# Performance work log

Hardware: AMD Instinct MI355X
Metric: run time of the kernel (lower is better)

The kernel has to match this reference:

```python
import jax, jax.numpy as jnp
import numpy as np

B, S, HID, H = 2, 2048, 1024, 16
D = HID // H
ROTARY_BASE = 10000.0
LN_EPS = 1e-5
NEG = -1e9


def setup_inputs() -> dict:
    key = jax.random.key(0)
    ks = jax.random.split(key, 20)
    w = lambda k, shape: (jax.random.normal(k, shape, jnp.float32) * 0.02)
    return {
        "x": jax.random.normal(ks[0], (B, S, HID), jnp.float32),
        "mask": jnp.ones((B, S), jnp.int32),
        "wq": w(ks[1], (HID, HID)), "bq": jnp.zeros((HID,), jnp.float32),
        "wk": w(ks[2], (HID, HID)), "bk": jnp.zeros((HID,), jnp.float32),
        "wv": w(ks[3], (HID, HID)), "bv": jnp.zeros((HID,), jnp.float32),
        "wo": w(ks[4], (HID, HID)), "bo": jnp.zeros((HID,), jnp.float32),
        "w1": w(ks[5], (HID, 4 * HID)), "b1": jnp.zeros((4 * HID,), jnp.float32),
        "w2": w(ks[6], (4 * HID, HID)), "b2": jnp.zeros((HID,), jnp.float32),
        "ln1_g": jnp.ones((HID,), jnp.float32), "ln1_b": jnp.zeros((HID,), jnp.float32),
        "ln2_g": jnp.ones((HID,), jnp.float32), "ln2_b": jnp.zeros((HID,), jnp.float32),
    }


def _layer_norm(z, g, b):
    m = z.mean(-1, keepdims=True)
    v = ((z - m) ** 2).mean(-1, keepdims=True)
    return (z - m) / jnp.sqrt(v + LN_EPS) * g + b


def _rope(t, cos, sin):
    # t: [B,H,S,D]; even/odd halves rotated then CONCATENATED (matches source, not interleaved)
    e, o = t[..., 0::2], t[..., 1::2]
    return jnp.concatenate([e * cos - o * sin, e * sin + o * cos], axis=-1)


def reference(x, mask, wq, bq, wk, bk, wv, bv, wo, bo, w1, b1, w2, b2,
              ln1_g, ln1_b, ln2_g, ln2_b):
    b, s, hid = x.shape
    h, d = H, D
    # rotary tables for positions [0, s)
    inv_freq = 1.0 / (ROTARY_BASE ** (jnp.arange(0, d, 2, dtype=jnp.float32) / d))
    freqs = jnp.arange(s, dtype=jnp.float32)[:, None] * inv_freq[None, :]  # [S, D/2]
    cos = jnp.cos(freqs)[None, None]  # [1,1,S,D/2]
    sin = jnp.sin(freqs)[None, None]

    # ---- attention sublayer (pre-norm) ----
    xn = _layer_norm(x, ln1_g, ln1_b)
    q = (xn @ wq + bq).reshape(b, s, h, d).transpose(0, 2, 1, 3)
    k = (xn @ wk + bk).reshape(b, s, h, d).transpose(0, 2, 1, 3)
    v = (xn @ wv + bv).reshape(b, s, h, d).transpose(0, 2, 1, 3)
    q = _rope(q, cos, sin)
    k = _rope(k, cos, sin)

    scores = jnp.einsum('bhqd,bhkd->bhqk', q, k) / np.sqrt(d).astype(np.float32)
    pad = (mask == 0)[:, None, None, :]              # [B,1,1,S]
    scores = jnp.where(pad, NEG, scores)
    causal = jnp.triu(jnp.ones((s, s), bool), 1)     # [S,S]
    scores = jnp.where(causal, NEG, scores)
    probs = jax.nn.softmax(scores, axis=-1)          # dropout p=0.0 (eval)
    ctx = jnp.einsum('bhqk,bhkd->bhqd', probs, v)
    ctx = ctx.transpose(0, 2, 1, 3).reshape(b, s, hid)
    attn_out = ctx @ wo + bo
    x = x + attn_out

    # ---- FFN sublayer (pre-norm) ----
    xn = _layer_norm(x, ln2_g, ln2_b)
    f = jax.nn.gelu(xn @ w1 + b1, approximate=True) @ w2 + b2
    return x + f
```

## Files before the change

### kernel.cpp

```cpp
#include <hip/hip_runtime.h>

typedef unsigned short u16;
typedef unsigned int u32;
typedef __attribute__((ext_vector_type(8))) u16 u16x8;
typedef __attribute__((ext_vector_type(4))) u16 u16x4;
typedef __attribute__((ext_vector_type(8))) __bf16 bf16x8;
typedef __attribute__((ext_vector_type(4))) float f32x4;

static __device__ __forceinline__ float bf2f(u16 u) {
    union { u32 i; float f; } v; v.i = ((u32)u) << 16; return v.f;
}
static __device__ __forceinline__ u16 f2bf(float f) {
    union { float f; u32 i; } v; v.f = f;
    u32 r = v.i + 0x7fffu + ((v.i >> 16) & 1u);
    return (u16)(r >> 16);
}
static __device__ __forceinline__ u16 f2bfn(float f) {
    __bf16 h = (__bf16)f;
    return *(u16*)&h;
}
static __device__ __forceinline__ void gl_lds16(const void* gsrc, void* ldst) {
    __builtin_amdgcn_global_load_lds((const __attribute__((address_space(1))) void*)gsrc,
                                     (__attribute__((address_space(3))) void*)ldst, 16, 0, 0);
}

__global__ __launch_bounds__(256) void transpose_cvt(const float* __restrict__ in,
                                                     u16* __restrict__ out, int K, int N) {
    __shared__ float t[32][33];
    int k0 = blockIdx.y << 5, n0 = blockIdx.x << 5;
    int r = threadIdx.x >> 3, c4 = threadIdx.x & 7;
    float4 v = *(const float4*)(in + (size_t)(k0 + r) * N + n0 + (c4 << 2));
    t[r][c4 * 4 + 0] = v.x; t[r][c4 * 4 + 1] = v.y;
    t[r][c4 * 4 + 2] = v.z; t[r][c4 * 4 + 3] = v.w;
    __syncthreads();
    u16x4 o;
    o[0] = f2bf(t[c4 * 4 + 0][r]); o[1] = f2bf(t[c4 * 4 + 1][r]);
    o[2] = f2bf(t[c4 * 4 + 2][r]); o[3] = f2bf(t[c4 * 4 + 3][r]);
    *(u16x4*)(out + (size_t)(n0 + r) * K + k0 + (c4 << 2)) = o;
}

__global__ void concat_bias(const float* __restrict__ bq, const float* __restrict__ bk,
                            const float* __restrict__ bv, float* __restrict__ bqkv) {
    int i = blockIdx.x * 256 + threadIdx.x;
    if (i < 3072) {
        float v = (i < 1024) ? bq[i] : (i < 2048 ? bk[i - 1024] : bv[i - 2048]);
        bqkv[i] = v;
    }
}

__global__ void rope_tab(float* __restrict__ cost, float* __restrict__ sint) {
    int idx = blockIdx.x * 256 + threadIdx.x;
    int s = idx >> 5, f = idx & 31;
    float inv = powf(10000.0f, -((float)(2 * f)) / 64.0f);
    float a = (float)s * inv;
    cost[idx] = cosf(a);
    sint[idx] = sinf(a);
}

__global__ __launch_bounds__(256) void ln_kernel(const float* __restrict__ x,
                                                 const float* __restrict__ gam,
                                                 const float* __restrict__ bet,
                                                 u16* __restrict__ out) {
    int row = blockIdx.x, tid = threadIdx.x;
    float4 v = *((const float4*)(x + (size_t)row * 1024) + tid);
    float s = v.x + v.y + v.z + v.w;
    float sq = v.x * v.x + v.y * v.y + v.z * v.z + v.w * v.w;
    #pragma unroll
    for (int off = 32; off >= 1; off >>= 1) {
        s += __shfl_xor(s, off);
        sq += __shfl_xor(sq, off);
    }
    __shared__ float red[8];
    int wid = tid >> 6, lane = tid & 63;
    if (lane == 0) { red[wid] = s; red[wid + 4] = sq; }
    __syncthreads();
    float ts = red[0] + red[1] + red[2] + red[3];
    float tq = red[4] + red[5] + red[6] + red[7];
    float mean = ts * (1.0f / 1024.0f);
    float var = tq * (1.0f / 1024.0f) - mean * mean;
    float rstd = rsqrtf(var + 1e-5f);
    float4 g = ((const float4*)gam)[tid];
    float4 b = ((const float4*)bet)[tid];
    u16x4 o;
    o[0] = f2bfn((v.x - mean) * rstd * g.x + b.x);
    o[1] = f2bfn((v.y - mean) * rstd * g.y + b.y);
    o[2] = f2bfn((v.z - mean) * rstd * g.z + b.z);
    o[3] = f2bfn((v.w - mean) * rstd * g.w + b.w);
    *(u16x4*)(out + (size_t)row * 1024 + (tid << 2)) = o;
}

template <int EPI>
__global__ __launch_bounds__(256) void gemm_bt(const u16* __restrict__ A, const u16* __restrict__ Bt,
                                               const float* __restrict__ bias,
                                               const float* __restrict__ res,
                                               u16* __restrict__ outb, float* __restrict__ outf,
                                               float* __restrict__ pout,
                                               int M, int N, int K) {
    __shared__ __align__(16) u16 As[3][4096];
    __shared__ __align__(16) u16 Bs[3][4096];
    const int tid = threadIdx.x;
    const int lane = tid & 63, wid = tid >> 6;
    const int g = lane >> 4, cl = lane & 15;
    const int wr = wid >> 1, wc = wid & 1;
    const int gx = gridDim.x;
    const int lid = blockIdx.y * gx + blockIdx.x;
    const int per8 = (gx * gridDim.y) >> 3;
    const int newlin = (lid & 7) * per8 + (lid >> 3);
    const int m0 = (newlin / gx) << 7;
    const int n0 = (newlin % gx) << 7;
    const int kchunk = K / gridDim.z;
    const int kbase = blockIdx.z * kchunk;
    const int NT = kchunk >> 5;
    f32x4 acc[4][4] = {};
    const int grow = tid >> 2;
    const int gcol = (tid & 3) ^ ((tid >> 3) & 3);

    auto stage = [&](int buf, int kt) {
        const int ko = kbase + (kt << 5);
        gl_lds16(A + (size_t)(m0 + grow) * K + ko + (gcol << 3),       &As[buf][wid << 9]);
        gl_lds16(A + (size_t)(m0 + grow + 64) * K + ko + (gcol << 3),  &As[buf][(wid << 9) + 2048]);
        gl_lds16(Bt + (size_t)(n0 + grow) * K + ko + (gcol << 3),      &Bs[buf][wid << 9]);
        gl_lds16(Bt + (size_t)(n0 + grow + 64) * K + ko + (gcol << 3), &Bs[buf][(wid << 9) + 2048]);
    };

    stage(0, 0);
    stage(1, 1);
    for (int kt = 0; kt < NT; ++kt) {
        if (kt + 1 < NT) asm volatile("s_waitcnt vmcnt(4)" ::: "memory");
        else             asm volatile("s_waitcnt vmcnt(0)" ::: "memory");
        __builtin_amdgcn_s_barrier();
        __builtin_amdgcn_sched_barrier(0);
        if (kt + 2 < NT) stage((kt + 2) % 3, kt + 2);
        const int cb = kt % 3;
        bf16x8 a[4], b[4];
        #pragma unroll
        for (int i = 0; i < 4; ++i) {
            int row = (wr << 6) + (i << 4) + cl;
            a[i] = *(const bf16x8*)&As[cb][((row << 2) + (g ^ ((row >> 1) & 3))) << 3];
        }
        #pragma unroll
        for (int j = 0; j < 4; ++j) {
            int row = (wc << 6) + (j << 4) + cl;
            b[j] = *(const bf16x8*)&Bs[cb][((row << 2) + (g ^ ((row >> 1) & 3))) << 3];
        }
        __builtin_amdgcn_s_setprio(1);
        #pragma unroll
        for (int i = 0; i < 4; ++i)
            #pragma unroll
            for (int j = 0; j < 4; ++j)
                acc[i][j] = __builtin_amdgcn_mfma_f32_16x16x32_bf16(a[i], b[j], acc[i][j], 0, 0, 0);
        __builtin_amdgcn_s_setprio(0);
    }
    if (blockIdx.z == 0) {
        #pragma unroll
        for (int i = 0; i < 4; ++i)
            #pragma unroll
            for (int j = 0; j < 4; ++j) {
                int row = m0 + (wr << 6) + (i << 4) + (g << 2);
                int col = n0 + (wc << 6) + (j << 4) + cl;
                float bc = bias[col];
                #pragma unroll
                for (int rr = 0; rr < 4; ++rr) {
                    float v = acc[i][j][rr] + bc;
                    size_t idx = (size_t)(row + rr) * N + col;
                    if constexpr (EPI == 0) {
                        outb[idx] = f2bfn(v);
                    } else if constexpr (EPI == 1) {
                        outf[idx] = v + res[idx];
                    } else {
                        float t = 0.7978845608f * (v + 0.044715f * v * v * v);
                        outb[idx] = f2bfn(v / (1.0f + exp2f(t * -2.88539008f)));
                    }
                }
            }
    } else {
        #pragma unroll
        for (int i = 0; i < 4; ++i)
            #pragma unroll
            for (int j = 0; j < 4; ++j) {
                int row = m0 + (wr << 6) + (i << 4) + (g << 2);
                int col = n0 + (wc << 6) + (j << 4) + cl;
                #pragma unroll
                for (int rr = 0; rr < 4; ++rr)
                    pout[(size_t)(row + rr) * N + col] = acc[i][j][rr];
            }
    }
}

__global__ __launch_bounds__(256) void reduce_add(float* __restrict__ out, const float* __restrict__ p) {
    int i = blockIdx.x * 256 + threadIdx.x;
    float4 a = ((const float4*)out)[i];
    float4 b = ((const float4*)p)[i];
    a.x += b.x; a.y += b.y; a.z += b.z; a.w += b.w;
    ((float4*)out)[i] = a;
}

__global__ __launch_bounds__(256) void rope_qk(const u16* __restrict__ qkv,
                                               const float* __restrict__ cost,
                                               const float* __restrict__ sint,
                                               u16* __restrict__ qr, u16* __restrict__ kr) {
    int tid = threadIdx.x;
    int rowid = (blockIdx.x << 4) + (tid >> 4);
    int j = tid & 15;
    int half = j >> 3, jj = j & 7;
    int b = rowid >> 15;
    int h = (rowid >> 11) & 15;
    int s = rowid & 2047;
    size_t qbase = (size_t)((b << 11) + s) * 3072 + (h << 6);
    float cf[4], sf_[4];
    {
        float4 c = *(const float4*)(cost + (s << 5) + (jj << 2));
        float4 sn = *(const float4*)(sint + (s << 5) + (jj << 2));
        cf[0] = c.x; cf[1] = c.y; cf[2] = c.z; cf[3] = c.w;
        sf_[0] = sn.x; sf_[1] = sn.y; sf_[2] = sn.z; sf_[3] = sn.w;
    }
    size_t obase = (size_t)rowid * 64 + (half << 5) + (jj << 2);
    {
        u16x8 v = *(const u16x8*)(qkv + qbase + (jj << 3));
        u16x4 o;
        #pragma unroll
        for (int m2 = 0; m2 < 4; ++m2) {
            float e = bf2f(v[2 * m2]), od = bf2f(v[2 * m2 + 1]);
            float val = (half == 0) ? (e * cf[m2] - od * sf_[m2]) : (e * sf_[m2] + od * cf[m2]);
            o[m2] = f2bfn(val * 0.1803368801f);
        }
        *(u16x4*)(qr + obase) = o;
    }
    {
        u16x8 v = *(const u16x8*)(qkv + qbase + 1024 + (jj << 3));
        u16x4 o;
        #pragma unroll
        for (int m2 = 0; m2 < 4; ++m2) {
            float e = bf2f(v[2 * m2]), od = bf2f(v[2 * m2 + 1]);
            float val = (half == 0) ? (e * cf[m2] - od * sf_[m2]) : (e * sf_[m2] + od * cf[m2]);
            o[m2] = f2bfn(val);
        }
        *(u16x4*)(kr + obase) = o;
    }
}

__global__ __launch_bounds__(256) void v_transpose(const u16* __restrict__ qkv,
                                                   u16* __restrict__ vt) {
    __shared__ __align__(16) u16 tl[64 * 80];
    int stile = blockIdx.x, bh = blockIdx.y;
    int b = bh >> 4, h = bh & 15;
    int tid = threadIdx.x;
    #pragma unroll
    for (int i = 0; i < 2; ++i) {
        int slot = tid + (i << 8);
        int srow = slot >> 3, c = slot & 7;
        u16x8 v = *(const u16x8*)(qkv + (size_t)((b << 11) + (stile << 6) + srow) * 3072 + 2048 + (h << 6) + (c << 3));
        *(u16x8*)(tl + srow * 80 + (c << 3)) = v;
    }
    __syncthreads();
    #pragma unroll
    for (int i = 0; i < 2; ++i) {
        int slot = tid + (i << 8);
        int drow = slot >> 3, c = slot & 7;
        u16x8 o;
        #pragma unroll
        for (int m2 = 0; m2 < 8; ++m2) o[m2] = tl[(c * 8 + m2) * 80 + drow];
        *(u16x8*)(vt + ((size_t)bh * 64 + drow) * 2048 + (stile << 6) + (c << 3)) = o;
    }
}

__global__ __launch_bounds__(256) void attn_kernel(const u16* __restrict__ Q, const u16* __restrict__ Kd,
                                                   const u16* __restrict__ Vt, const int* __restrict__ mask,
                                                   u16* __restrict__ ctx) {
    __shared__ __align__(16) u16 Ks[2][4096];
    __shared__ __align__(16) u16 Vs[2][4096];
    __shared__ __align__(16) u16 Ps[4096];
    const int tid = threadIdx.x, lane = tid & 63, w = tid >> 6;
    const int g = lane >> 4, cl = lane & 15;
    const int pair = blockIdx.x, bh = blockIdx.y;
    const int b = bh >> 4, h = bh & 15;
    const u16* Kb = Kd + (size_t)bh * 2048 * 64;
    const u16* Vb = Vt + (size_t)bh * 64 * 2048;
    const int srow0 = tid >> 3, sc0 = tid & 7;
    const int srow1 = (tid + 256) >> 3, sc1 = sc0;
    bf16x8 onesb;
    #pragma unroll
    for (int i2 = 0; i2 < 8; ++i2) onesb[i2] = (__bf16)1.0f;

    #pragma unroll
    for (int ci = 0; ci < 2; ++ci) {
        const int qb = (ci == 0) ? (31 - pair) : pair;
        const size_t qoff = ((size_t)bh * 2048 + qb * 64 + w * 16 + cl) * 64;
        const bf16x8 qa0 = *(const bf16x8*)(Q + qoff + (g << 3));
        const bf16x8 qa1 = *(const bf16x8*)(Q + qoff + 32 + (g << 3));
        const int qrow_base = qb * 64 + w * 16 + g * 4;
        f32x4 acc[4] = {};
        f32x4 lsum = {};

        u16x8 k0a = *(const u16x8*)(Kb + (size_t)srow0 * 64 + (sc0 << 3));
        u16x8 k0b = *(const u16x8*)(Kb + (size_t)srow1 * 64 + (sc1 << 3));
        u16x8 v0a = *(const u16x8*)(Vb + (size_t)srow0 * 2048 + (sc0 << 3));
        u16x8 v0b = *(const u16x8*)(Vb + (size_t)srow1 * 2048 + (sc1 << 3));
        __syncthreads();
        *(u16x8*)((char*)&Ks[0][0] + srow0 * 128 + ((sc0 ^ (srow0 & 7)) << 4)) = k0a;
        *(u16x8*)((char*)&Ks[0][0] + srow1 * 128 + ((sc1 ^ (srow1 & 7)) << 4)) = k0b;
        *(u16x8*)((char*)&Vs[0][0] + srow0 * 128 + ((sc0 ^ (srow0 & 7)) << 4)) = v0a;
        *(u16x8*)((char*)&Vs[0][0] + srow1 * 128 + ((sc1 ^ (srow1 & 7)) << 4)) = v0b;
        __syncthreads();

        int cur = 0;
        for (int t = 0; t <= qb; ++t) {
            const bool more = (t < qb);
            u16x8 rka, rkb, rva, rvb;
            if (more) {
                const u16* Kg = Kb + (size_t)(t + 1) * 64 * 64;
                rka = *(const u16x8*)(Kg + (size_t)srow0 * 64 + (sc0 << 3));
                rkb = *(const u16x8*)(Kg + (size_t)srow1 * 64 + (sc1 << 3));
                rva = *(const u16x8*)(Vb + (size_t)srow0 * 2048 + (t + 1) * 64 + (sc0 << 3));
                rvb = *(const u16x8*)(Vb + (size_t)srow1 * 2048 + (t + 1) * 64 + (sc1 << 3));
            }
            f32x4 sf[4];
            __builtin_amdgcn_s_setprio(1);
            #pragma unroll
            for (int ct = 0; ct < 4; ++ct) {
                f32x4 s = {};
                int krow = ct * 16 + cl;
                bf16x8 kb0 = *(const bf16x8*)((char*)&Ks[cur][0] + krow * 128 + ((g ^ (krow & 7)) << 4));
                bf16x8 kb1 = *(const bf16x8*)((char*)&Ks[cur][0] + krow * 128 + (((4 + g) ^ (krow & 7)) << 4));
                s = __builtin_amdgcn_mfma_f32_16x16x32_bf16(qa0, kb0, s, 0, 0, 0);
                s = __builtin_amdgcn_mfma_f32_16x16x32_bf16(qa1, kb1, s, 0, 0, 0);
                sf[ct] = s;
            }
            __builtin_amdgcn_s_setprio(0);
            const bool diag = (t == qb);
            #pragma unroll
            for (int ct = 0; ct < 4; ++ct) {
                int kcol = t * 64 + ct * 16 + cl;
                float mvf = (float)mask[(b << 11) + kcol];
                #pragma unroll
                for (int rr = 0; rr < 4; ++rr) {
                    float p = exp2f(sf[ct][rr]) * mvf;
                    if (diag) p = (kcol <= qrow_base + rr) ? p : 0.0f;
                    int prow = g * 4 + rr, pcol = ct * 16 + cl;
                    *(u16*)((char*)Ps + w * 2048 + prow * 128 + (((pcol >> 3) ^ (prow & 7)) << 4) + ((pcol & 7) << 1)) = f2bfn(p);
                }
            }
            __builtin_amdgcn_s_setprio(1);
            #pragma unroll
            for (int kc = 0; kc < 2; ++kc) {
                bf16x8 pa = *(const bf16x8*)((char*)Ps + w * 2048 + cl * 128 + (((kc * 4 + g) ^ (cl & 7)) << 4));
                lsum = __builtin_amdgcn_mfma_f32_16x16x32_bf16(pa, onesb, lsum, 0, 0, 0);
                #pragma unroll
                for (int n = 0; n < 4; ++n) {
                    int vrow = n * 16 + cl;
                    bf16x8 vb = *(const bf16x8*)((char*)&Vs[cur][0] + vrow * 128 + (((kc * 4 + g) ^ (vrow & 7)) << 4));
                    acc[n] = __builtin_amdgcn_mfma_f32_16x16x32_bf16(pa, vb, acc[n], 0, 0, 0);
                }
            }
            __builtin_amdgcn_s_setprio(0);
            if (more) {
                *(u16x8*)((char*)&Ks[cur ^ 1][0] + srow0 * 128 + ((sc0 ^ (srow0 & 7)) << 4)) = rka;
                *(u16x8*)((char*)&Ks[cur ^ 1][0] + srow1 * 128 + ((sc1 ^ (srow1 & 7)) << 4)) = rkb;
                *(u16x8*)((char*)&Vs[cur ^ 1][0] + srow0 * 128 + ((sc0 ^ (srow0 & 7)) << 4)) = rva;
                *(u16x8*)((char*)&Vs[cur ^ 1][0] + srow1 * 128 + ((sc1 ^ (srow1 & 7)) << 4)) = rvb;
                __syncthreads();
            }
            cur ^= 1;
        }
        #pragma unroll
        for (int n = 0; n < 4; ++n)
            #pragma unroll
            for (int rr = 0; rr < 4; ++rr) {
                int token = (b << 11) + qb * 64 + w * 16 + g * 4 + rr;
                int col = (h << 6) + n * 16 + cl;
                ctx[(size_t)token * 1024 + col] = f2bfn(acc[n][rr] / lsum[rr]);
            }
    }
}

extern "C" void kernel_launch(void* const* d_in, const int* in_sizes, int n_in,
                              void* d_out, int out_size, void* d_ws, size_t ws_size,
                              hipStream_t stream) {
    const float* x   = (const float*)d_in[0];
    const int* mask  = (const int*)d_in[1];
    const float* wq  = (const float*)d_in[2];
    const float* bq  = (const float*)d_in[3];
    const float* wk  = (const float*)d_in[4];
    const float* bk  = (const float*)d_in[5];
    const float* wv  = (const float*)d_in[6];
    const float* bv  = (const float*)d_in[7];
    const float* wo  = (const float*)d_in[8];
    const float* bo  = (const float*)d_in[9];
    const float* w1  = (const float*)d_in[10];
    const float* b1  = (const float*)d_in[11];
    const float* w2  = (const float*)d_in[12];
    const float* b2  = (const float*)d_in[13];
    const float* g1  = (const float*)d_in[14];
    const float* be1 = (const float*)d_in[15];
    const float* g2  = (const float*)d_in[16];
    const float* be2 = (const float*)d_in[17];
    float* out = (float*)d_out;
    char* ws = (char*)d_ws;

    u16* wqkvT  = (u16*)(ws + 0);
    u16* woT    = (u16*)(ws + 6291456);
    u16* w1T    = (u16*)(ws + 8388608);
    u16* w2T    = (u16*)(ws + 16777216);
    float* bqkv = (float*)(ws + 25165824);
    float* cost = (float*)(ws + 25178112);
    float* sint = (float*)(ws + 25440256);
    u16* xn     = (u16*)(ws + 25702400);
    float* x2   = (float*)(ws + 34091008);
    u16* qkv    = (u16*)(ws + 50868224);
    u16* ffh    = (u16*)(ws + 50868224);
    u16* qr     = (u16*)(ws + 76034048);
    u16* kr     = (u16*)(ws + 84422656);
    u16* vt     = (u16*)(ws + 92811264);
    float* part = (float*)(ws + 84422656);
    u16* ctx    = (u16*)(ws + 101199872);

    transpose_cvt<<<dim3(32, 32), 256, 0, stream>>>(wq, wqkvT, 1024, 1024);
    transpose_cvt<<<dim3(32, 32), 256, 0, stream>>>(wk, wqkvT + 1024 * 1024, 1024, 1024);
    transpose_cvt<<<dim3(32, 32), 256, 0, stream>>>(wv, wqkvT + 2048 * 1024, 1024, 1024);
    transpose_cvt<<<dim3(32, 32), 256, 0, stream>>>(wo, woT, 1024, 1024);
    transpose_cvt<<<dim3(128, 32), 256, 0, stream>>>(w1, w1T, 1024, 4096);
    transpose_cvt<<<dim3(32, 128), 256, 0, stream>>>(w2, w2T, 4096, 1024);
    concat_bias<<<12, 256, 0, stream>>>(bq, bk, bv, bqkv);
    rope_tab<<<256, 256, 0, stream>>>(cost, sint);

    ln_kernel<<<4096, 256, 0, stream>>>(x, g1, be1, xn);
    gemm_bt<0><<<dim3(24, 32, 1), 256, 0, stream>>>(xn, wqkvT, bqkv, nullptr, qkv, nullptr, nullptr, 4096, 3072, 1024);
    rope_qk<<<4096, 256, 0, stream>>>(qkv, cost, sint, qr, kr);
    v_transpose<<<dim3(32, 32), 256, 0, stream>>>(qkv, vt);
    attn_kernel<<<dim3(16, 32), 256, 0, stream>>>(qr, kr, vt, mask, ctx);
    gemm_bt<1><<<dim3(8, 32, 2), 256, 0, stream>>>(ctx, woT, bo, x, nullptr, x2, part, 4096, 1024, 1024);
    reduce_add<<<4096, 256, 0, stream>>>(x2, part);
    ln_kernel<<<4096, 256, 0, stream>>>(x2, g2, be2, xn);
    gemm_bt<2><<<dim3(32, 32, 1), 256, 0, stream>>>(xn, w1T, b1, nullptr, ffh, nullptr, nullptr, 4096, 4096, 1024);
    gemm_bt<1><<<dim3(8, 32, 2), 256, 0, stream>>>(ffh, w2T, b2, x2, nullptr, out, part, 4096, 1024, 4096);
    reduce_add<<<4096, 256, 0, stream>>>(out, part);
}
```

Measured before the change: 289.5 us.

## Add 256x256-tile 512-thread GEMM for QKV and FFN-up projections

Adds a new GEMM kernel with 256x256 output tiles, 8 waves, a double-buffered 128KB LDS stage with XOR swizzle, and loads for the next K-tile spread across the four compute sub-steps. The QKV and W1 projections now use it in place of the 128x128 gemm_bt, and gemm_bt keeps only its residual epilogue. Larger tiles raise arithmetic intensity and cut global and LDS traffic per FLOP. In exchange the grid shrinks to 192 and 256 blocks, which may underfill the 256 CUs, and register pressure rises because each thread holds 32 accumulators.

New measurement: 278.1 us. -3.9%, faster.

```diff
diff --git a/kernel.cpp b/kernel.cpp
--- a/kernel.cpp
+++ b/kernel.cpp
@@ -87,6 +87,109 @@
     o[2] = f2bfn((v.z - mean) * rstd * g.z + b.z);
     o[3] = f2bfn((v.w - mean) * rstd * g.w + b.w);
     *(u16x4*)(out + (size_t)row * 1024 + (tid << 2)) = o;
+}
+
+template <int EPI>
+__global__ __launch_bounds__(512, 2) void gemm256(const u16* __restrict__ A, const u16* __restrict__ Bt,
+                                                  const float* __restrict__ bias,
+                                                  u16* __restrict__ outb, int M, int N, int K) {
+    __shared__ __align__(16) u16 lds[65536];
+    const int tid = threadIdx.x;
+    const int lane = tid & 63, wid = tid >> 6;
+    const int cl = lane & 15, g4 = lane >> 4;
+    const int wr = wid >> 2, wc = wid & 3;
+    const int gx = gridDim.x;
+    const int lid = blockIdx.y * gx + blockIdx.x;
+    const int per8 = (gx * gridDim.y) >> 3;
+    const int newlin = (lid & 7) * per8 + (lid >> 3);
+    const int m0 = (newlin / gx) << 8;
+    const int n0 = (newlin % gx) << 8;
+    const int NT = K >> 6;
+    f32x4 acc[8][4] = {};
+    const int r0 = tid >> 3;          const int gc0 = (tid & 7) ^ (r0 & 7);
+    const int r1 = (tid + 512) >> 3;  const int gc1 = (tid & 7) ^ (r1 & 7);
+    const int wub = wid << 10;
+
+    auto stageHalf = [&](int buf, int mat, int h, int kt) {
+        const u16* src = mat ? Bt : A;
+        const int base0 = mat ? n0 : m0;
+        char* db = (char*)lds + buf * 131072 / 2 * 0 + 0;
+        (void)db;
+        char* d = (char*)lds + buf * 65536 + mat * 32768 + h * 16384 + wub;
+        gl_lds16(src + (size_t)(base0 + h * 128 + r0) * K + (kt << 6) + (gc0 << 3), d);
+        gl_lds16(src + (size_t)(base0 + h * 128 + r1) * K + (kt << 6) + (gc1 << 3), d + 8192);
+    };
+
+    stageHalf(0, 0, 0, 0); stageHalf(0, 0, 1, 0);
+    stageHalf(0, 1, 0, 0); stageHalf(0, 1, 1, 0);
+    asm volatile("s_waitcnt vmcnt(0)" ::: "memory");
+    __builtin_amdgcn_s_barrier();
+
+    for (int t = 0; t < NT; ++t) {
+        const int buf = t & 1, nbuf = buf ^ 1;
+        const bool more = (t + 1 < NT);
+        const int abase = buf * 65536 + wr * 16384;
+        const int bbase = buf * 65536 + 32768 + (wc >> 1) * 16384;
+        bf16x8 bfr[4][2];
+        #pragma unroll
+        for (int q = 0; q < 4; ++q) {
+            bf16x8 afr[2][2];
+            #pragma unroll
+            for (int di = 0; di < 2; ++di)
+                #pragma unroll
+                for (int ks = 0; ks < 2; ++ks) {
+                    int row = q * 32 + di * 16 + cl;
+                    int gr = ks * 4 + g4;
+                    afr[di][ks] = *(const bf16x8*)((char*)lds + abase + (((row << 3) + (gr ^ (row & 7))) << 4));
+                }
+            if (q == 0) {
+                #pragma unroll
+                for (int j = 0; j < 4; ++j)
+                    #pragma unroll
+                    for (int ks = 0; ks < 2; ++ks) {
+                        int row = ((wc & 1) << 6) + j * 16 + cl;
+                        int gr = ks * 4 + g4;
+                        bfr[j][ks] = *(const bf16x8*)((char*)lds + bbase + (((row << 3) + (gr ^ (row & 7))) << 4));
+                    }
+            }
+            if (more) stageHalf(nbuf, q >> 1, q & 1, t + 1);
+            __builtin_amdgcn_s_barrier();
+            asm volatile("s_waitcnt lgkmcnt(0)" ::: "memory");
+            __builtin_amdgcn_sched_barrier(0);
+            __builtin_amdgcn_s_setprio(1);
+            #pragma unroll
+            for (int di = 0; di < 2; ++di)
+                #pragma unroll
+                for (int j = 0; j < 4; ++j)
+                    #pragma unroll
+                    for (int ks = 0; ks < 2; ++ks)
+                        acc[q * 2 + di][j] = __builtin_amdgcn_mfma_f32_16x16x32_bf16(
+                            afr[di][ks], bfr[j][ks], acc[q * 2 + di][j], 0, 0, 0);
+            __builtin_amdgcn_s_setprio(0);
+            if (q == 3 && more) asm volatile("s_waitcnt vmcnt(0)" ::: "memory");
+            __builtin_amdgcn_s_barrier();
+            if (q == 3) __builtin_amdgcn_sched_barrier(0);
+        }
+    }
+    #pragma unroll
+    for (int i = 0; i < 8; ++i)
+        #pragma unroll
+        for (int j = 0; j < 4; ++j) {
+            int row = m0 + wr * 128 + i * 16 + g4 * 4;
+            int col = n0 + wc * 64 + j * 16 + cl;
+            float bc = bias[col];
+            #pragma unroll
+            for (int rr = 0; rr < 4; ++rr) {
+                float v = acc[i][j][rr] + bc;
+                size_t idx = (size_t)(row + rr) * N + col;
+                if constexpr (EPI == 0) {
+                    outb[idx] = f2bfn(v);
+                } else {
+                    float tg = 0.7978845608f * (v + 0.044715f * v * v * v);
+                    outb[idx] = f2bfn(v / (1.0f + exp2f(tg * -2.88539008f)));
+                }
+            }
+        }
 }
 
 template <int EPI>
@@ -163,14 +266,7 @@
                 for (int rr = 0; rr < 4; ++rr) {
                     float v = acc[i][j][rr] + bc;
                     size_t idx = (size_t)(row + rr) * N + col;
-                    if constexpr (EPI == 0) {
-                        outb[idx] = f2bfn(v);
-                    } else if constexpr (EPI == 1) {
-                        outf[idx] = v + res[idx];
-                    } else {
-                        float t = 0.7978845608f * (v + 0.044715f * v * v * v);
-                        outb[idx] = f2bfn(v / (1.0f + exp2f(t * -2.88539008f)));
-                    }
+                    outf[idx] = v + res[idx];
                 }
             }
     } else {
@@ -424,14 +520,14 @@
     rope_tab<<<256, 256, 0, stream>>>(cost, sint);
 
     ln_kernel<<<4096, 256, 0, stream>>>(x, g1, be1, xn);
-    gemm_bt<0><<<dim3(24, 32, 1), 256, 0, stream>>>(xn, wqkvT, bqkv, nullptr, qkv, nullptr, nullptr, 4096, 3072, 1024);
+    gemm256<0><<<dim3(12, 16), 512, 0, stream>>>(xn, wqkvT, bqkv, qkv, 4096, 3072, 1024);
     rope_qk<<<4096, 256, 0, stream>>>(qkv, cost, sint, qr, kr);
     v_transpose<<<dim3(32, 32), 256, 0, stream>>>(qkv, vt);
     attn_kernel<<<dim3(16, 32), 256, 0, stream>>>(qr, kr, vt, mask, ctx);
     gemm_bt<1><<<dim3(8, 32, 2), 256, 0, stream>>>(ctx, woT, bo, x, nullptr, x2, part, 4096, 1024, 1024);
     reduce_add<<<4096, 256, 0, stream>>>(x2, part);
     ln_kernel<<<4096, 256, 0, stream>>>(x2, g2, be2, xn);
-    gemm_bt<2><<<dim3(32, 32, 1), 256, 0, stream>>>(xn, w1T, b1, nullptr, ffh, nullptr, nullptr, 4096, 4096, 1024);
+    gemm256<2><<<dim3(16, 16), 512, 0, stream>>>(xn, w1T, b1, ffh, 4096, 4096, 1024);
     gemm_bt<1><<<dim3(8, 32, 2), 256, 0, stream>>>(ffh, w2T, b2, x2, nullptr, out, part, 4096, 1024, 4096);
     reduce_add<<<4096, 256, 0, stream>>>(out, part);
 }
```
